# Kernel optimization log

Measured on AMD Instinct MI355X. Metric: run time of the kernel, lower is better.

Reference implementation:

```python
import jax, jax.numpy as jnp
import numpy as np


def conv2d(x, w, b):
    # NCHW input, OIHW kernel, SAME padding, stride 1
    y = jax.lax.conv_general_dilated(x, w, (1, 1), 'SAME',
                                     dimension_numbers=('NCHW', 'OIHW', 'NCHW'))
    return y + b[None, :, None, None]


def maxpool2(x):
    return jax.lax.reduce_window(x, -jnp.inf, jax.lax.max,
                                 (1, 1, 2, 2), (1, 1, 2, 2), 'VALID')


def gelu(x):
    return jax.nn.gelu(x, approximate=False)  # torch default exact GELU


def up2(x):
    # nearest-neighbor upsample x2 (torch Upsample mode='nearest')
    return jnp.repeat(jnp.repeat(x, 2, axis=2), 2, axis=3)


DIM = 32
CODEBOOK_SIZE = 512
COMMIT_W = 1.0


def setup_inputs() -> dict:
    key = jax.random.key(0)
    ks = jax.random.split(key, 10)
    s = 0.1
    return {
        'x': jax.random.normal(ks[0], (32, 1, 256, 256), jnp.float32),
        'e1_w': jax.random.normal(ks[1], (16, 1, 3, 3), jnp.float32) * s,
        'e1_b': jnp.zeros((16,), jnp.float32),
        'e2_w': jax.random.normal(ks[2], (32, 16, 3, 3), jnp.float32) * s,
        'e2_b': jnp.zeros((32,), jnp.float32),
        'codebook': jax.random.normal(ks[3], (CODEBOOK_SIZE, DIM), jnp.float32),
        'd1_w': jax.random.normal(ks[4], (16, 32, 3, 3), jnp.float32) * s,
        'd1_b': jnp.zeros((16,), jnp.float32),
        'd2_w': jax.random.normal(ks[5], (1, 16, 3, 3), jnp.float32) * s,
        'd2_b': jnp.zeros((1,), jnp.float32),
    }


def reference(x, e1_w, e1_b, e2_w, e2_b, codebook, d1_w, d1_b, d2_w, d2_b):
    # ---- encoder ----
    h = conv2d(x, e1_w, e1_b)
    h = maxpool2(h)
    h = gelu(h)
    h = conv2d(h, e2_w, e2_b)
    h = maxpool2(h)                      # [B, 32, H/4, W/4]

    # ---- vector quantize (accept_image_fmap=True) ----
    B, C, H, W = h.shape
    flat = h.transpose(0, 2, 3, 1).reshape(-1, C)          # [N, C] tokens
    # squared euclidean distances to codebook
    d = ((flat * flat).sum(-1, keepdims=True)
         - 2.0 * flat @ codebook.T
         + (codebook * codebook).sum(-1))                   # [N, K]
    idx = jnp.argmin(d, axis=-1)                            # [N] int
    q = codebook[idx]                                       # gather [N, C]
    commit_loss = COMMIT_W * jnp.mean((jax.lax.stop_gradient(q) - flat) ** 2)
    # straight-through estimator
    q = flat + jax.lax.stop_gradient(q - flat)
    hq = q.reshape(B, H, W, C).transpose(0, 3, 1, 2)        # back to NCHW
    indices = idx.reshape(B, H, W)

    # ---- decoder ----
    y = up2(hq)
    y = conv2d(y, d1_w, d1_b)
    y = gelu(y)
    y = up2(y)
    y = conv2d(y, d2_w, d2_b)
    return jnp.clip(y, -1.0, 1.0), indices, commit_loss
```

## Files before the change

kernel.cpp:

```cpp
#include <hip/hip_runtime.h>
#include <math.h>

#define GELU(v) (0.5f * (v) * (1.0f + erff((v)*0.70710678118654752440f)))

typedef __attribute__((ext_vector_type(8))) short short8;
typedef __attribute__((ext_vector_type(4))) float f32x4;
typedef __attribute__((ext_vector_type(16))) float f32x16;
#define MFMA16 __builtin_amdgcn_mfma_f32_16x16x32_bf16
#define MFMA32 __builtin_amdgcn_mfma_f32_32x32x16_bf16

#define SPLIT3(V, U1, U2, U3)                                                  \
  unsigned U1 = __float_as_uint(V) & 0xFFFF0000u;                              \
  float _r1 = (V)-__uint_as_float(U1);                                         \
  unsigned U2 = __float_as_uint(_r1) & 0xFFFF0000u;                            \
  float _r2 = _r1 - __uint_as_float(U2);                                       \
  unsigned U3 = __float_as_uint(_r2) & 0xFFFF0000u;

__global__ __launch_bounds__(256) void k_fold(const float* __restrict__ e2w,
                                              const float* __restrict__ d1w,
                                              const float* __restrict__ d2w,
                                              const float* __restrict__ cb,
                                              float* __restrict__ fwd2,
                                              unsigned short* __restrict__ cbs,
                                              float* __restrict__ csqg,
                                              unsigned short* __restrict__ wfrag,
                                              unsigned short* __restrict__ wfd1) {
  int i = blockIdx.x * 256 + threadIdx.x;
  if (i < 256) {
    int j = i;
    int pt = j & 15, ic = j >> 4;
    int a = pt >> 3, b2 = (pt >> 2) & 1, dy = (pt >> 1) & 1, dx = pt & 1;
    const float* wsrc = d2w + ic * 9;
    float s = 0.f;
    for (int ky = 0; ky < 3; ++ky) {
      int rm = (a == 0) ? (ky == 0 ? 0 : 1) : (ky == 2 ? 1 : 0);
      if (rm != dy) continue;
      for (int kx = 0; kx < 3; ++kx) {
        int cm = (b2 == 0) ? (kx == 0 ? 0 : 1) : (kx == 2 ? 1 : 0);
        if (cm == dx) s += wsrc[ky * 3 + kx];
      }
    }
    fwd2[j] = s;
  } else if (i < 16640) {
    int j = i - 256;
    float v = cb[j];
    SPLIT3(v, u1, u2, u3)
    cbs[j] = (unsigned short)(u1 >> 16);
    cbs[16384 + j] = (unsigned short)(u2 >> 16);
    cbs[32768 + j] = (unsigned short)(u3 >> 16);
  } else if (i < 17152) {
    int c = i - 16640;
    const float* row = cb + (size_t)c * 32;
    float s = 0.f;
#pragma unroll
    for (int d = 0; d < 32; ++d) s = fmaf(row[d], row[d], s);
    csqg[c] = s;
  } else if (i < 30976) {
    int j = i - 17152;
    int p = j / 4608, rem = j - p * 4608;
    int t = rem >> 9, l2 = (rem >> 3) & 63, jj = rem & 7;
    float v = e2w[((l2 & 31) * 16 + ((l2 >> 5) * 8 + jj)) * 9 + t];
    SPLIT3(v, u1, u2, u3)
    unsigned short r = (p == 0)   ? (unsigned short)(u1 >> 16)
                       : (p == 1) ? (unsigned short)(u2 >> 16)
                                  : (unsigned short)(u3 >> 16);
    wfrag[j] = r;
  } else if (i < 86272) {
    int j = i - 30976;
    int slot = j >> 9, l2 = (j >> 3) & 63, jj = j & 7;
    int cx = slot / 36, rem = slot % 36;
    int r3 = rem / 12, rem2 = rem % 12;
    int kh = rem2 / 6, rem3 = rem2 % 6;
    int pp = rem3 / 3, part = rem3 % 3;
    int c = l2 & 31, hi = l2 >> 5;
    int oc = c & 15, b2 = c >> 4;
    int ic = kh * 16 + hi * 8 + jj;
    int dy = r3 - pp, dx = cx - b2;
    float s = 0.f;
    if ((unsigned)dy < 2u && (unsigned)dx < 2u) {
      const float* wsrc = d1w + (oc * 32 + ic) * 9;
      for (int ky = 0; ky < 3; ++ky) {
        int rm = (pp == 0) ? (ky == 0 ? 0 : 1) : (ky == 2 ? 1 : 0);
        if (rm != dy) continue;
        for (int kx = 0; kx < 3; ++kx) {
          int cm = (b2 == 0) ? (kx == 0 ? 0 : 1) : (kx == 2 ? 1 : 0);
          if (cm == dx) s += wsrc[ky * 3 + kx];
        }
      }
    }
    SPLIT3(s, u1, u2, u3)
    unsigned short r = (part == 0)   ? (unsigned short)(u1 >> 16)
                       : (part == 1) ? (unsigned short)(u2 >> 16)
                                     : (unsigned short)(u3 >> 16);
    wfd1[j] = r;
  }
}

__global__ __launch_bounds__(256) void k_enc1(const float* __restrict__ x,
                                              const float* __restrict__ w,
                                              const float* __restrict__ bias,
                                              float* __restrict__ h1) {
  int gid = blockIdx.x * 256 + threadIdx.x;
  int xx = gid & 127, yy = (gid >> 7) & 127, b = gid >> 14;
  const float* xp = x + (size_t)b * 65536;
  int r0 = 2 * yy - 1, c0 = 2 * xx - 1;
  float in[4][4];
#pragma unroll
  for (int i = 0; i < 4; ++i) {
    int r = r0 + i;
    bool rv = (unsigned)r < 256u;
#pragma unroll
    for (int j = 0; j < 4; ++j) {
      int c = c0 + j;
      in[i][j] = (rv && (unsigned)c < 256u) ? xp[r * 256 + c] : 0.0f;
    }
  }
  float vout[16];
#pragma unroll
  for (int oc = 0; oc < 16; ++oc) {
    const float* wp = w + oc * 9;
    float s00 = 0.f, s01 = 0.f, s10 = 0.f, s11 = 0.f;
#pragma unroll
    for (int ky = 0; ky < 3; ++ky)
#pragma unroll
      for (int kx = 0; kx < 3; ++kx) {
        float wv = wp[ky * 3 + kx];
        s00 = fmaf(in[ky][kx], wv, s00);
        s01 = fmaf(in[ky][kx + 1], wv, s01);
        s10 = fmaf(in[ky + 1][kx], wv, s10);
        s11 = fmaf(in[ky + 1][kx + 1], wv, s11);
      }
    float m = fmaxf(fmaxf(s00, s01), fmaxf(s10, s11)) + bias[oc];
    vout[oc] = GELU(m);
  }
  float* op = h1 + (size_t)b * 262144 + ((size_t)yy * 128 + xx) * 16;
#pragma unroll
  for (int q = 0; q < 4; ++q) {
    float4 vq;
    vq.x = vout[4 * q + 0]; vq.y = vout[4 * q + 1];
    vq.z = vout[4 * q + 2]; vq.w = vout[4 * q + 3];
    *(float4*)(op + 4 * q) = vq;
  }
}

__global__ __launch_bounds__(256) void k_enc2(const float* __restrict__ h1,
                                              const unsigned short* __restrict__ wfrag,
                                              const float* __restrict__ bias,
                                              float* __restrict__ h2) {
  __shared__ __align__(16) unsigned short sA[3 * 2 * 10 * 34 * 8];
  const int PP = 2 * 10 * 34 * 8;
  int tid = threadIdx.x;
  int b = blockIdx.y;
  int X0 = (blockIdx.x & 3) * 32, Y0 = (blockIdx.x >> 2) * 8;
  const float* ip = h1 + (size_t)b * 262144;
  for (int i = tid; i < 5440; i += 256) {
    int yy = i / 544, rem = i % 544, xx = rem >> 4, ic = rem & 15;
    int y = Y0 - 1 + yy, xg = X0 - 1 + xx;
    float v = ((unsigned)y < 128u && (unsigned)xg < 128u)
                  ? ip[((size_t)y * 128 + xg) * 16 + ic] : 0.f;
    SPLIT3(v, u1, u2, u3)
    int si = (((ic >> 3) * 10 + yy) * 34 + xx) * 8 + (ic & 7);
    sA[si] = (unsigned short)(u1 >> 16);
    sA[PP + si] = (unsigned short)(u2 >> 16);
    sA[2 * PP + si] = (unsigned short)(u3 >> 16);
  }
  __syncthreads();

  int l = tid & 63, w = tid >> 6;
  int xl = l & 31, ich = l >> 5;
  f32x16 acc0[2], acc1[2];
#pragma unroll
  for (int s = 0; s < 2; ++s)
#pragma unroll
    for (int r = 0; r < 16; ++r) { acc0[s][r] = 0.f; acc1[s][r] = 0.f; }

#pragma unroll
  for (int t = 0; t < 9; ++t) {
    int dy = t / 3, dx = t % 3;
    int s = t & 1;
    const unsigned short* wb = wfrag + t * 512 + l * 8;
    short8 bf1 = *(const short8*)(wb);
    short8 bf2 = *(const short8*)(wb + 4608);
    short8 bf3 = *(const short8*)(wb + 9216);
    int g0 = ((ich * 10) + (2 * w + dy)) * 34 + xl + dx;
    const unsigned short* a0p = sA + g0 * 8;
    short8 a01 = *(const short8*)(a0p);
    short8 a02 = *(const short8*)(a0p + PP);
    short8 a03 = *(const short8*)(a0p + 2 * PP);
    const unsigned short* a1p = a0p + 34 * 8;
    short8 a11 = *(const short8*)(a1p);
    short8 a12 = *(const short8*)(a1p + PP);
    short8 a13 = *(const short8*)(a1p + 2 * PP);
    acc0[s] = MFMA32(a01, bf1, acc0[s], 0, 0, 0);
    acc0[s] = MFMA32(a01, bf2, acc0[s], 0, 0, 0);
    acc0[s] = MFMA32(a02, bf1, acc0[s], 0, 0, 0);
    acc0[s] = MFMA32(a02, bf2, acc0[s], 0, 0, 0);
    acc0[s] = MFMA32(a01, bf3, acc0[s], 0, 0, 0);
    acc0[s] = MFMA32(a03, bf1, acc0[s], 0, 0, 0);
    acc1[s] = MFMA32(a11, bf1, acc1[s], 0, 0, 0);
    acc1[s] = MFMA32(a11, bf2, acc1[s], 0, 0, 0);
    acc1[s] = MFMA32(a12, bf1, acc1[s], 0, 0, 0);
    acc1[s] = MFMA32(a12, bf2, acc1[s], 0, 0, 0);
    acc1[s] = MFMA32(a11, bf3, acc1[s], 0, 0, 0);
    acc1[s] = MFMA32(a13, bf1, acc1[s], 0, 0, 0);
  }

  float bv = bias[l & 31];
  int ypool = (Y0 >> 1) + w;
  float* op = h2 + (size_t)b * 131072 + (size_t)(l & 31) * 4096 + ypool * 64 + (X0 >> 1);
#pragma unroll
  for (int k = 0; k < 8; ++k) {
    float e0 = (acc0[0][2 * k] + acc0[1][2 * k]);
    float o0 = (acc0[0][2 * k + 1] + acc0[1][2 * k + 1]);
    float e1 = (acc1[0][2 * k] + acc1[1][2 * k]);
    float o1 = (acc1[0][2 * k + 1] + acc1[1][2 * k + 1]);
    float m = fmaxf(fmaxf(e0, o0), fmaxf(e1, o1)) + bv;
    int row = ((2 * k) & 3) + 8 * ((2 * k) >> 2) + 4 * ich;
    op[row >> 1] = m;
  }
}

__global__ __launch_bounds__(256) void k_vq(const float* __restrict__ h2,
                                            const unsigned short* __restrict__ cbs,
                                            const float* __restrict__ csqg,
                                            float* __restrict__ idxout,
                                            float* __restrict__ partial) {
  __shared__ __align__(16) unsigned short sA[3 * 256 * 40];
  __shared__ float sFsq[256];
  __shared__ float sBd[256];
  __shared__ int sBi[256];
  __shared__ float sred[4];
  int tid = threadIdx.x;
  int blk = blockIdx.x;
  int t0 = blk * 256;
  size_t abase = (size_t)(t0 >> 12) * 131072 + (t0 & 4095);

  {
    const float* src = h2 + abase + tid;
    float fsq = 0.f;
#pragma unroll
    for (int g = 0; g < 4; ++g) {
      short8 p1, p2, p3;
#pragma unroll
      for (int e = 0; e < 8; ++e) {
        float v = src[(g * 8 + e) * 4096];
        fsq = fmaf(v, v, fsq);
        SPLIT3(v, u1, u2, u3)
        p1[e] = (short)(u1 >> 16);
        p2[e] = (short)(u2 >> 16);
        p3[e] = (short)(u3 >> 16);
      }
      *(short8*)(sA + (0 * 256 + tid) * 40 + g * 8) = p1;
      *(short8*)(sA + (1 * 256 + tid) * 40 + g * 8) = p2;
      *(short8*)(sA + (2 * 256 + tid) * 40 + g * 8) = p3;
    }
    sFsq[tid] = fsq;
  }
  __syncthreads();

  int l = tid & 63, w = tid >> 6;
  int cl = l & 15, k0 = (l >> 4) * 8;
  short8 af[3][4];
#pragma unroll
  for (int p = 0; p < 3; ++p)
#pragma unroll
    for (int tq = 0; tq < 4; ++tq) {
      int tok = w * 64 + tq * 16 + cl;
      af[p][tq] = *(const short8*)(sA + (p * 256 + tok) * 40 + k0);
    }

  float bd[4][4];
  int bi[4][4];
#pragma unroll
  for (int a = 0; a < 4; ++a)
#pragma unroll
    for (int b = 0; b < 4; ++b) { bd[a][b] = 3.4e38f; bi[a][b] = 0; }

#define LOADB(S, CT)                                                           \
  {                                                                            \
    int col = (CT)*16 + cl;                                                    \
    b1##S = *(const short8*)(cbs + (0 * 512 + col) * 32 + k0);                 \
    b2##S = *(const short8*)(cbs + (1 * 512 + col) * 32 + k0);                 \
    b3##S = *(const short8*)(cbs + (2 * 512 + col) * 32 + k0);                 \
    cq##S = csqg[col];                                                         \
  }
#define COMPUTE(S, CT)                                                         \
  {                                                                            \
    _Pragma("unroll") for (int tq = 0; tq < 4; ++tq) {                         \
      f32x4 acc = {0.f, 0.f, 0.f, 0.f};                                        \
      acc = MFMA16(af[0][tq], b1##S, acc, 0, 0, 0);                            \
      acc = MFMA16(af[0][tq], b2##S, acc, 0, 0, 0);                            \
      acc = MFMA16(af[1][tq], b1##S, acc, 0, 0, 0);                            \
      acc = MFMA16(af[1][tq], b2##S, acc, 0, 0, 0);                            \
      acc = MFMA16(af[0][tq], b3##S, acc, 0, 0, 0);                            \
      acc = MFMA16(af[2][tq], b1##S, acc, 0, 0, 0);                            \
      _Pragma("unroll") for (int i = 0; i < 4; ++i) {                          \
        float d = fmaf(-2.f, acc[i], cq##S);                                   \
        if (d < bd[tq][i]) { bd[tq][i] = d; bi[tq][i] = (CT)*16 + cl; }        \
      }                                                                        \
    }                                                                          \
  }

  short8 b1A, b2A, b3A, b1B, b2B, b3B;
  float cqA, cqB;
  LOADB(A, 0)
  LOADB(B, 1)
#pragma unroll 1
  for (int ct = 0; ct < 32; ct += 2) {
    COMPUTE(A, ct)
    LOADB(A, (ct + 2) & 31)
    COMPUTE(B, ct + 1)
    LOADB(B, (ct + 3) & 31)
  }
#undef LOADB
#undef COMPUTE

#pragma unroll
  for (int tq = 0; tq < 4; ++tq)
#pragma unroll
    for (int i = 0; i < 4; ++i)
#pragma unroll
      for (int m = 1; m < 16; m <<= 1) {
        float od = __shfl_xor(bd[tq][i], m, 64);
        int ob = __shfl_xor(bi[tq][i], m, 64);
        if (od < bd[tq][i] || (od == bd[tq][i] && ob < bi[tq][i])) {
          bd[tq][i] = od;
          bi[tq][i] = ob;
        }
      }
  if (cl == 0) {
#pragma unroll
    for (int tq = 0; tq < 4; ++tq)
#pragma unroll
      for (int i = 0; i < 4; ++i) {
        int tokl = w * 64 + tq * 16 + (l >> 4) * 4 + i;
        sBi[tokl] = bi[tq][i];
        sBd[tokl] = bd[tq][i];
      }
  }
  __syncthreads();

  idxout[t0 + tid] = (float)sBi[tid];
  float loss = sBd[tid] + sFsq[tid];
#pragma unroll
  for (int off = 32; off > 0; off >>= 1) loss += __shfl_down(loss, off, 64);
  if (l == 0) sred[w] = loss;
  __syncthreads();
  if (tid == 0) partial[blk] = (sred[0] + sred[1]) + (sred[2] + sred[3]);
}

__global__ __launch_bounds__(256) void k_loss(const float* __restrict__ partial,
                                              float* __restrict__ lossout) {
  __shared__ float sred[4];
  int tid = threadIdx.x;
  float v = partial[tid] + partial[tid + 256];
#pragma unroll
  for (int off = 32; off > 0; off >>= 1) v += __shfl_down(v, off, 64);
  if ((tid & 63) == 0) sred[tid >> 6] = v;
  __syncthreads();
  if (tid == 0)
    lossout[0] = ((sred[0] + sred[1]) + (sred[2] + sred[3])) * (1.0f / 4194304.0f);
}

__global__ __launch_bounds__(256, 2) void k_dec1(const float* __restrict__ idxf,
                                                 const unsigned short* __restrict__ cbs,
                                                 const unsigned short* __restrict__ wfd1,
                                                 const float* __restrict__ bias,
                                                 float* __restrict__ o) {
  __shared__ __align__(16) unsigned short sA[3 * 12240];
  __shared__ int sIdx[340];
  const int PP = 12240;
  int tid = threadIdx.x;
  int b = blockIdx.y;
  int qx0 = (blockIdx.x & 1) * 32, qy0 = (blockIdx.x >> 1) * 8;
  const float* ib = idxf + (size_t)b * 4096;
  for (int i = tid; i < 340; i += 256) {
    int yy = i / 34, xx = i % 34;
    int y = qy0 - 1 + yy, x = qx0 - 1 + xx;
    sIdx[i] = ((unsigned)y < 64u && (unsigned)x < 64u) ? (int)ib[y * 64 + x] : -1;
  }
  __syncthreads();
  for (int i = tid; i < 4080; i += 256) {
    int pos = i / 12, sub = i % 12, part = sub >> 2, g = sub & 3;
    int idx = sIdx[pos];
    short8 v = {0, 0, 0, 0, 0, 0, 0, 0};
    if (idx >= 0) v = *(const short8*)(cbs + ((part << 9) + idx) * 32 + g * 8);
    *(short8*)(sA + part * PP + pos * 36 + g * 8) = v;
  }
  __syncthreads();

  int l = tid & 63, w = tid >> 6;
  int xl = l & 31, hi = l >> 5;
  f32x16 acc[2][2];
#pragma unroll
  for (int s = 0; s < 2; ++s)
#pragma unroll
    for (int p2 = 0; p2 < 2; ++p2)
#pragma unroll
      for (int r = 0; r < 16; ++r) acc[s][p2][r] = 0.f;

#pragma unroll
  for (int cx = 0; cx < 3; ++cx) {
    short8 Bf[4][2][3];
#pragma unroll
    for (int q = 0; q < 4; ++q) {
      int r3 = (q == 0) ? 0 : (q == 3) ? 2 : 1;
      int pq = (q >= 2) ? 1 : 0;
#pragma unroll
      for (int kh = 0; kh < 2; ++kh)
#pragma unroll
        for (int pt = 0; pt < 3; ++pt) {
          int slot = cx * 36 + r3 * 12 + kh * 6 + pq * 3 + pt;
          Bf[q][kh][pt] = *(const short8*)(wfd1 + (size_t)slot * 512 + l * 8);
        }
    }
#pragma unroll
    for (int ar = 0; ar < 4; ++ar) {
#pragma unroll
      for (int kh = 0; kh < 2; ++kh) {
        const unsigned short* ap =
            sA + ((2 * w + ar) * 34 + xl + cx) * 36 + kh * 16 + hi * 8;
        short8 a1 = *(const short8*)(ap);
        short8 a2 = *(const short8*)(ap + PP);
        short8 a3 = *(const short8*)(ap + 2 * PP);
#pragma unroll
        for (int s = 0; s < 2; ++s) {
          int ry = ar - s;
          if (ry < 0 || ry > 2) continue;
#pragma unroll
          for (int p2 = 0; p2 < 2; ++p2) {
            if ((ry == 0 && p2 == 1) || (ry == 2 && p2 == 0)) continue;
            int q = ry + p2;
            f32x16 t = acc[s][p2];
            t = MFMA32(a1, Bf[q][kh][0], t, 0, 0, 0);
            t = MFMA32(a1, Bf[q][kh][1], t, 0, 0, 0);
            t = MFMA32(a2, Bf[q][kh][0], t, 0, 0, 0);
            t = MFMA32(a2, Bf[q][kh][1], t, 0, 0, 0);
            t = MFMA32(a1, Bf[q][kh][2], t, 0, 0, 0);
            t = MFMA32(a3, Bf[q][kh][0], t, 0, 0, 0);
            acc[s][p2] = t;
          }
        }
      }
    }
  }

  float bv = bias[l & 15];
  int b2 = (l >> 4) & 1;
  float* ob = o + (size_t)b * 262144 + (size_t)(l & 15) * 16384 + (qx0 << 1) + b2;
#pragma unroll
  for (int s = 0; s < 2; ++s) {
    int qy = qy0 + 2 * w + s;
#pragma unroll
    for (int p2 = 0; p2 < 2; ++p2) {
      int Y = 2 * qy + p2;
      float* op = ob + Y * 128;
#pragma unroll
      for (int reg = 0; reg < 16; ++reg) {
        int rowval = (reg & 3) + 8 * (reg >> 2) + 4 * hi;
        op[2 * rowval] = GELU(acc[s][p2][reg] + bv);
      }
    }
  }
}

__global__ __launch_bounds__(256) void k_dec2(const float* __restrict__ d1,
                                              const float* __restrict__ fwd2,
                                              const float* __restrict__ bias,
                                              float* __restrict__ out) {
  __shared__ float st[16 * 360];
  int tid = threadIdx.x;
  int b = blockIdx.y;
  int R0 = (blockIdx.x >> 3) * 16, C0 = (blockIdx.x & 7) * 16;
  const float* ip = d1 + (size_t)b * 262144;
  for (int i = tid; i < 5184; i += 256) {
    int ic = i / 324, rr = (i % 324) / 18, cc = i % 18;
    int r = R0 - 1 + rr, c = C0 - 1 + cc;
    st[ic * 360 + rr * 20 + cc] =
        ((unsigned)r < 128u && (unsigned)c < 128u) ? ip[ic * 16384 + r * 128 + c] : 0.f;
  }
  __syncthreads();
  int lane = tid & 63, wid = tid >> 6;
  int qy = wid >> 1, qx = wid & 1;
  int ty = qy * 8 + (lane >> 3), tx = qx * 8 + (lane & 7);
  float acc[4] = {0.f, 0.f, 0.f, 0.f};
#pragma unroll 1
  for (int ic = 0; ic < 16; ++ic) {
    const float* t = st + ic * 360 + ty * 20 + tx;
    float i3[3][3];
#pragma unroll
    for (int dy = 0; dy < 3; ++dy)
#pragma unroll
      for (int dx = 0; dx < 3; ++dx) i3[dy][dx] = t[dy * 20 + dx];
    const float* wp = fwd2 + ic * 16;
#pragma unroll
    for (int p = 0; p < 4; ++p) {
      int a = p >> 1, b2 = p & 1;
#pragma unroll
      for (int tp = 0; tp < 4; ++tp) {
        int dy = tp >> 1, dx = tp & 1;
        acc[p] = fmaf(i3[a + dy][b2 + dx], wp[p * 4 + tp], acc[p]);
      }
    }
  }
  float bv = bias[0];
  int Y = 2 * (R0 + ty), X = 2 * (C0 + tx);
  float* op = out + (size_t)b * 65536 + Y * 256 + X;
  float2 r0v, r1v;
  r0v.x = fminf(1.0f, fmaxf(-1.0f, acc[0] + bv));
  r0v.y = fminf(1.0f, fmaxf(-1.0f, acc[1] + bv));
  r1v.x = fminf(1.0f, fmaxf(-1.0f, acc[2] + bv));
  r1v.y = fminf(1.0f, fmaxf(-1.0f, acc[3] + bv));
  *(float2*)op = r0v;
  *(float2*)(op + 256) = r1v;
}

extern "C" void kernel_launch(void* const* d_in, const int* in_sizes, int n_in,
                              void* d_out, int out_size, void* d_ws, size_t ws_size,
                              hipStream_t stream) {
  const float* x   = (const float*)d_in[0];
  const float* e1w = (const float*)d_in[1];
  const float* e1b = (const float*)d_in[2];
  const float* e2w = (const float*)d_in[3];
  const float* e2b = (const float*)d_in[4];
  const float* cb  = (const float*)d_in[5];
  const float* d1w = (const float*)d_in[6];
  const float* d1b = (const float*)d_in[7];
  const float* d2w = (const float*)d_in[8];
  const float* d2b = (const float*)d_in[9];

  float* out = (float*)d_out;
  float* y       = out;
  float* idxout  = out + 2097152;
  float* lossout = out + 2097152 + 131072;

  float* ws = (float*)d_ws;
  float* h1      = ws;
  float* h2      = ws + 8388608;
  float* partial = ws + 12582912;
  float* fwd2    = ws + 12596224;
  float* d1o     = h1;

  unsigned short* cbs = (unsigned short*)out;
  float* csqg = out + 24576;
  unsigned short* wfrag = (unsigned short*)(out + 25088);
  unsigned short* wfd1 = (unsigned short*)(out + 32000);

  k_fold<<<dim3(337), 256, 0, stream>>>(e2w, d1w, d2w, cb, fwd2, cbs, csqg, wfrag, wfd1);
  k_enc1<<<dim3(2048), 256, 0, stream>>>(x, e1w, e1b, h1);
  k_enc2<<<dim3(64, 32), 256, 0, stream>>>(h1, wfrag, e2b, h2);
  k_vq<<<dim3(512), 256, 0, stream>>>(h2, cbs, csqg, idxout, partial);
  k_loss<<<dim3(1), 256, 0, stream>>>(partial, lossout);
  k_dec1<<<dim3(16, 32), 256, 0, stream>>>(idxout, cbs, wfd1, d1b, d1o);
  k_dec2<<<dim3(64, 32), 256, 0, stream>>>(d1o, fwd2, d2b, y);
}
```

Before: 242.5 us.

## Remap enc1/enc2 block indices for XCD-local halo reuse and vectorize enc2 staging

Block indices of k_enc1 and k_enc2 are remapped so blocks assigned round-robin to the same XCD work on neighbouring row bands. Halo rows written by enc1 and reread by enc2 should then stay in the local L2. The enc2 shared-memory staging loop now reads 8 channels per thread with float4 loads and writes the three bf16 split planes as short8 vector stores, replacing scalar loads, divides and 2-byte stores. The new mapping relies on the assumption that consecutive block IDs rotate across 8 XCDs.

New measurement: 227.4 us. -6.2%, faster.

```diff
diff --git a/kernel.cpp b/kernel.cpp
--- a/kernel.cpp
+++ b/kernel.cpp
@@ -100,8 +100,11 @@
                                               const float* __restrict__ w,
                                               const float* __restrict__ bias,
                                               float* __restrict__ h1) {
-  int gid = blockIdx.x * 256 + threadIdx.x;
-  int xx = gid & 127, yy = (gid >> 7) & 127, b = gid >> 14;
+  int n = blockIdx.x;
+  int ysl = n & 7, m = n >> 3;
+  int b = m & 31, k = m >> 5;
+  int yy = ysl * 16 + k * 2 + (threadIdx.x >> 7);
+  int xx = threadIdx.x & 127;
   const float* xp = x + (size_t)b * 65536;
   int r0 = 2 * yy - 1, c0 = 2 * xx - 1;
   float in[4][4];
@@ -130,8 +133,8 @@
         s10 = fmaf(in[ky + 1][kx], wv, s10);
         s11 = fmaf(in[ky + 1][kx + 1], wv, s11);
       }
-    float m = fmaxf(fmaxf(s00, s01), fmaxf(s10, s11)) + bias[oc];
-    vout[oc] = GELU(m);
+    float mm = fmaxf(fmaxf(s00, s01), fmaxf(s10, s11)) + bias[oc];
+    vout[oc] = GELU(mm);
   }
   float* op = h1 + (size_t)b * 262144 + ((size_t)yy * 128 + xx) * 16;
 #pragma unroll
@@ -150,19 +153,36 @@
   __shared__ __align__(16) unsigned short sA[3 * 2 * 10 * 34 * 8];
   const int PP = 2 * 10 * 34 * 8;
   int tid = threadIdx.x;
-  int b = blockIdx.y;
-  int X0 = (blockIdx.x & 3) * 32, Y0 = (blockIdx.x >> 2) * 8;
+  int n = blockIdx.x;
+  int xcd = n & 7, m = n >> 3;
+  int ty = xcd * 2 + (m & 1);
+  int q0 = m >> 1;
+  int b = q0 >> 2, xt = q0 & 3;
+  int X0 = xt * 32, Y0 = ty * 8;
   const float* ip = h1 + (size_t)b * 262144;
-  for (int i = tid; i < 5440; i += 256) {
-    int yy = i / 544, rem = i % 544, xx = rem >> 4, ic = rem & 15;
+  for (int g = tid; g < 680; g += 256) {
+    int pos = g >> 1, ich = g & 1;
+    int yy = pos / 34, xx = pos - yy * 34;
     int y = Y0 - 1 + yy, xg = X0 - 1 + xx;
-    float v = ((unsigned)y < 128u && (unsigned)xg < 128u)
-                  ? ip[((size_t)y * 128 + xg) * 16 + ic] : 0.f;
-    SPLIT3(v, u1, u2, u3)
-    int si = (((ic >> 3) * 10 + yy) * 34 + xx) * 8 + (ic & 7);
-    sA[si] = (unsigned short)(u1 >> 16);
-    sA[PP + si] = (unsigned short)(u2 >> 16);
-    sA[2 * PP + si] = (unsigned short)(u3 >> 16);
+    float4 v0 = {0.f, 0.f, 0.f, 0.f}, v1 = {0.f, 0.f, 0.f, 0.f};
+    if ((unsigned)y < 128u && (unsigned)xg < 128u) {
+      const float* sp = ip + ((size_t)y * 128 + xg) * 16 + ich * 8;
+      v0 = *(const float4*)(sp);
+      v1 = *(const float4*)(sp + 4);
+    }
+    float vv[8] = {v0.x, v0.y, v0.z, v0.w, v1.x, v1.y, v1.z, v1.w};
+    short8 p1, p2, p3;
+#pragma unroll
+    for (int e = 0; e < 8; ++e) {
+      SPLIT3(vv[e], u1, u2, u3)
+      p1[e] = (short)(u1 >> 16);
+      p2[e] = (short)(u2 >> 16);
+      p3[e] = (short)(u3 >> 16);
+    }
+    int si = ((ich * 10 + yy) * 34 + xx) * 8;
+    *(short8*)(sA + si) = p1;
+    *(short8*)(sA + PP + si) = p2;
+    *(short8*)(sA + 2 * PP + si) = p3;
   }
   __syncthreads();
 
@@ -214,9 +234,9 @@
     float o0 = (acc0[0][2 * k + 1] + acc0[1][2 * k + 1]);
     float e1 = (acc1[0][2 * k] + acc1[1][2 * k]);
     float o1 = (acc1[0][2 * k + 1] + acc1[1][2 * k + 1]);
-    float m = fmaxf(fmaxf(e0, o0), fmaxf(e1, o1)) + bv;
+    float mm = fmaxf(fmaxf(e0, o0), fmaxf(e1, o1)) + bv;
     int row = ((2 * k) & 3) + 8 * ((2 * k) >> 2) + 4 * ich;
-    op[row >> 1] = m;
+    op[row >> 1] = mm;
   }
 }
 
@@ -548,7 +568,7 @@
 
   k_fold<<<dim3(337), 256, 0, stream>>>(e2w, d1w, d2w, cb, fwd2, cbs, csqg, wfrag, wfd1);
   k_enc1<<<dim3(2048), 256, 0, stream>>>(x, e1w, e1b, h1);
-  k_enc2<<<dim3(64, 32), 256, 0, stream>>>(h1, wfrag, e2b, h2);
+  k_enc2<<<dim3(2048), 256, 0, stream>>>(h1, wfrag, e2b, h2);
   k_vq<<<dim3(512), 256, 0, stream>>>(h2, cbs, csqg, idxout, partial);
   k_loss<<<dim3(1), 256, 0, stream>>>(partial, lossout);
   k_dec1<<<dim3(16, 32), 256, 0, stream>>>(idxout, cbs, wfd1, d1b, d1o);
```
